# Kernel optimization log

Hardware: AMD Instinct MI355X
Metric: run time of the kernel (lower is better)

The kernel has to match this reference:

```python
import jax, jax.numpy as jnp
import numpy as np

N_HEAD = 16
LN_EPS = 1e-5


def _layernorm(x, g, b):
    mu = jnp.mean(x, axis=-1, keepdims=True)
    var = jnp.mean(jnp.square(x - mu), axis=-1, keepdims=True)
    return (x - mu) * jax.lax.rsqrt(var + LN_EPS) * g + b


def setup_inputs() -> dict:
    key = jax.random.key(0)
    ks = jax.random.split(key, 12)
    B, S, D = 2, 2048, 1024
    F = 4 * D
    std = 0.02
    return {
        "x": jax.random.normal(ks[0], (B, S, D), jnp.float32),
        "w_attn": jax.random.normal(ks[1], (D, 3 * D), jnp.float32) * std,
        "b_attn": jnp.zeros((3 * D,), jnp.float32),
        "w_o": jax.random.normal(ks[2], (D, D), jnp.float32) * std,
        "b_o": jnp.zeros((D,), jnp.float32),
        "ln1_g": jnp.ones((D,), jnp.float32),
        "ln1_b": jnp.zeros((D,), jnp.float32),
        "w_fc": jax.random.normal(ks[3], (D, F), jnp.float32) * std,
        "b_fc": jnp.zeros((F,), jnp.float32),
        "w_pr": jax.random.normal(ks[4], (F, D), jnp.float32) * std,
        "b_pr": jnp.zeros((D,), jnp.float32),
        "ln2_g": jnp.ones((D,), jnp.float32),
        "ln2_b": jnp.zeros((D,), jnp.float32),
    }


def reference(x, w_attn, b_attn, w_o, b_o, ln1_g, ln1_b,
              w_fc, b_fc, w_pr, b_pr, ln2_g, ln2_b):
    B, S, D = x.shape
    H = N_HEAD
    hd = D // H

    # --- attention ---
    qkv = x @ w_attn + b_attn                      # [B,S,3D]
    q, k, v = jnp.split(qkv, 3, axis=-1)
    q = q.reshape(B, S, H, hd).transpose(0, 2, 1, 3)  # [B,H,S,hd]
    k = k.reshape(B, S, H, hd).transpose(0, 2, 1, 3)
    v = v.reshape(B, S, H, hd).transpose(0, 2, 1, 3)

    # scores in fp32, scaled by sqrt(head_dim) (scale=True)
    w = jnp.einsum('bhqd,bhkd->bhqk', q.astype(jnp.float32),
                   k.astype(jnp.float32)) / jnp.sqrt(jnp.float32(hd))
    bias = jnp.tril(jnp.ones((S, S), jnp.float32))     # causal mask slice of registered buffer
    w = w * bias + (-10000.0) * (1.0 - bias)
    a = jax.nn.softmax(w, axis=-1).astype(v.dtype)
    o = jnp.einsum('bhqk,bhkd->bhqd', a, v)            # [B,H,S,hd]
    o = o.transpose(0, 2, 1, 3).reshape(B, S, D)
    a_out = o @ w_o + b_o

    # --- post-LN residual + MLP (gelu, d_ff = 4D) ---
    n = _layernorm(x + a_out, ln1_g, ln1_b)
    m = jax.nn.gelu(n @ w_fc + b_fc, approximate=False) @ w_pr + b_pr
    h = _layernorm(n + m, ln2_g, ln2_b)
    return h
```

## Files before the change

kernel.cpp:

```cpp
#include <hip/hip_runtime.h>
#include <stdint.h>
#include <math.h>


typedef __attribute__((ext_vector_type(4))) float f32x4;
typedef __attribute__((ext_vector_type(8))) short s16x8;

__device__ __forceinline__ float bf2f(short s){
  unsigned u = ((unsigned)(unsigned short)s) << 16;
  return __builtin_bit_cast(float, u);
}
__device__ __forceinline__ short f2bf(float f){
  unsigned u = __builtin_bit_cast(unsigned, f);
  unsigned r = (u + 0x7fffu + ((u >> 16) & 1u)) >> 16;
  return (short)(unsigned short)r;
}

__device__ __forceinline__ void gload_lds16(const void* gp, void* lp){
  __builtin_amdgcn_global_load_lds(
      (__attribute__((address_space(1))) void*)const_cast<void*>(gp),
      (__attribute__((address_space(3))) void*)lp,
      16, 0, 0);
}

__global__ void cvt_f32_bf16(const float* __restrict__ in, short* __restrict__ out, int n){
  int i = (blockIdx.x * blockDim.x + threadIdx.x) * 4;
  if (i < n){
    float4 v = *(const float4*)(in + i);
    short4 o;
    o.x = f2bf(v.x); o.y = f2bf(v.y); o.z = f2bf(v.z); o.w = f2bf(v.w);
    *(short4*)(out + i) = o;
  }
}

__global__ __launch_bounds__(256) void wtrans(const float* __restrict__ in,
                                              short* __restrict__ out, int R, int C){
  __shared__ float tile[32][33];
  int c0 = blockIdx.x * 32, r0 = blockIdx.y * 32;
  int tx = threadIdx.x, ty = threadIdx.y;
  #pragma unroll
  for (int j = 0; j < 4; ++j)
    tile[ty + j*8][tx] = in[(size_t)(r0 + ty + j*8) * C + c0 + tx];
  __syncthreads();
  #pragma unroll
  for (int j = 0; j < 4; ++j)
    out[(size_t)(c0 + ty + j*8) * R + r0 + tx] = f2bf(tile[tx][ty + j*8]);
}

__global__ __launch_bounds__(256) void vtrans(const short* __restrict__ qkv,
                                              short* __restrict__ vt){
  __shared__ short tile[32][33];
  int bh = blockIdx.z; int b = bh >> 4, h = bh & 15;
  int s0 = blockIdx.x * 32, d0 = blockIdx.y * 32;
  int tx = threadIdx.x, ty = threadIdx.y;
  #pragma unroll
  for (int j = 0; j < 4; ++j)
    tile[ty + j*8][tx] = qkv[(size_t)(b*2048 + s0 + ty + j*8) * 3072 + 2048 + h*64 + d0 + tx];
  __syncthreads();
  #pragma unroll
  for (int j = 0; j < 4; ++j)
    vt[(size_t)(bh*64 + d0 + ty + j*8) * 2048 + s0 + tx] = tile[tx][ty + j*8];
}

#define GBM 128
#define GBN 128
#define GBK 64

__global__ __launch_bounds__(256, 4) void gemm_bf16(
    const short* __restrict__ A, const short* __restrict__ BT,
    const float* __restrict__ bias,
    void* __restrict__ out, void* __restrict__ out2,
    void* __restrict__ out3, void* __restrict__ out4,
    int M, int N, int K, int EPI, int KS)
{
  __shared__ short sA[GBM * GBK];
  __shared__ short sB[GBN * GBK];
  const int t = threadIdx.x;
  const int lane = t & 63;
  const int w = t >> 6;
  const int wr = w >> 1, wc = w & 1;
  const int lrow = lane & 15;
  const int lk = lane >> 4;

  const int gx = gridDim.x;
  const int nwg = gx * gridDim.y;
  const int P = blockIdx.y * gx + blockIdx.x;
  const int wg = (P & 7) * (nwg >> 3) + (P >> 3);
  const int m0 = (wg / gx) * GBM, n0 = (wg % gx) * GBN;

  const int Kspl = K / KS;
  const int kbeg = blockIdx.z * Kspl;

  f32x4 acc[4][4] = {};

  for (int kk = kbeg; kk < kbeg + Kspl; kk += GBK){
    __syncthreads();
    #pragma unroll
    for (int r = 0; r < 4; ++r){
      int o = r * 4096 + t * 16;
      int row = o >> 7;
      int phys = (o >> 4) & 7;
      int lsl = phys ^ (row & 7);
      gload_lds16(A + (size_t)(m0 + row) * K + kk + lsl * 8, (char*)sA + o);
    }
    #pragma unroll
    for (int r = 0; r < 4; ++r){
      int o = r * 4096 + t * 16;
      int row = o >> 7;
      int phys = (o >> 4) & 7;
      int lsl = phys ^ (row & 7);
      gload_lds16(BT + (size_t)(n0 + row) * K + kk + lsl * 8, (char*)sB + o);
    }
    __syncthreads();

    #pragma unroll
    for (int kc = 0; kc < 2; ++kc){
      s16x8 af[4], bf[4];
      #pragma unroll
      for (int rt = 0; rt < 4; ++rt){
        int row = wr*64 + rt*16 + lrow;
        int slot = (kc*4 + lk) ^ (row & 7);
        af[rt] = *(const s16x8*)&sA[row*64 + slot*8];
      }
      #pragma unroll
      for (int ct = 0; ct < 4; ++ct){
        int row = wc*64 + ct*16 + lrow;
        int slot = (kc*4 + lk) ^ (row & 7);
        bf[ct] = *(const s16x8*)&sB[row*64 + slot*8];
      }
      #pragma unroll
      for (int rt = 0; rt < 4; ++rt)
        #pragma unroll
        for (int ct = 0; ct < 4; ++ct)
          acc[rt][ct] = __builtin_amdgcn_mfma_f32_16x16x32_bf16(af[rt], bf[ct], acc[rt][ct], 0, 0, 0);
    }
  }

  void* pz = (blockIdx.z == 0) ? out : (blockIdx.z == 1) ? out2
           : (blockIdx.z == 2) ? out3 : out4;
  #pragma unroll
  for (int rt = 0; rt < 4; ++rt){
    #pragma unroll
    for (int ct = 0; ct < 4; ++ct){
      #pragma unroll
      for (int r = 0; r < 4; ++r){
        int row = m0 + wr*64 + rt*16 + lk*4 + r;
        int col = n0 + wc*64 + ct*16 + lrow;
        size_t idx = (size_t)row * N + col;
        if (EPI == 4){
          ((short*)pz)[idx] = f2bf(acc[rt][ct][r]);
        } else {
          float v = acc[rt][ct][r] + bias[col];
          if (EPI == 0){
            ((short*)out)[idx] = f2bf(v);
          } else {
            float g = 0.5f * v * (1.0f + erff(v * 0.70710678118654752f));
            ((short*)out)[idx] = f2bf(g);
          }
        }
      }
    }
  }
}

__global__ __launch_bounds__(256, 2) void attn_kernel(
    const short* __restrict__ qkv, const short* __restrict__ vt,
    short* __restrict__ ob)
{
  const int P = blockIdx.x;
  const int xcd = P & 7;
  const int idx = P >> 3;
  const int pairi = idx & 15;
  const int bh = xcd + ((idx >> 4) << 3);
  const int b = bh >> 4, h = bh & 15;
  const int t  = threadIdx.x;
  const int lane = t & 63;
  const int w = t >> 6;
  const int lrow = lane & 15, lk = lane >> 4;

  __shared__ short sK[2][64*64];
  __shared__ short sV[2][64*64];
  __shared__ short sP[4][16][68];

  const size_t kgbase = (size_t)(b*2048)*3072 + 1024 + h*64;
  const size_t vgbase = (size_t)((b*16 + h)*64)*2048;

  s16x8 bones;
  #pragma unroll
  for (int i = 0; i < 8; ++i) bones[i] = (short)0x3F80;

  auto stage = [&](int buf, int k0){
    #pragma unroll
    for (int r2 = 0; r2 < 2; ++r2){
      int o = r2*4096 + t*16;
      int row = o >> 7;
      int lsl = ((o >> 4) & 7) ^ (row & 7);
      gload_lds16(qkv + kgbase + (size_t)(k0 + row)*3072 + lsl*8, (char*)sK[buf] + o);
      gload_lds16(vt  + vgbase + (size_t)row*2048 + k0   + lsl*8, (char*)sV[buf] + o);
    }
  };

  for (int pass = 0; pass < 2; ++pass){
    const int qt = pass ? 31 - pairi : pairi;
    const int q0 = qt * 64;
    const int qbase = q0 + w * 16;

    s16x8 aq[2];
    #pragma unroll
    for (int kc = 0; kc < 2; ++kc)
      aq[kc] = *(const s16x8*)(qkv + (size_t)(b*2048 + qbase + lrow)*3072 + h*64 + kc*32 + lk*8);

    f32x4 oacc[4] = {};
    f32x4 sumacc = {};

    const int nt = qt + 1;
    __syncthreads();
    stage(0, 0);
    __syncthreads();
    int cur = 0;

    for (int ktile = 0; ktile < nt; ++ktile){
      const int k0 = ktile * 64;
      if (ktile + 1 < nt) stage(cur ^ 1, k0 + 64);

      f32x4 sacc[4] = {};
      __builtin_amdgcn_s_setprio(1);
      #pragma unroll
      for (int kc = 0; kc < 2; ++kc){
        #pragma unroll
        for (int ct = 0; ct < 4; ++ct){
          int row = ct*16 + lrow;
          int slot = (kc*4 + lk) ^ (row & 7);
          s16x8 bk = *(const s16x8*)&sK[cur][row*64 + slot*8];
          sacc[ct] = __builtin_amdgcn_mfma_f32_16x16x32_bf16(aq[kc], bk, sacc[ct], 0, 0, 0);
        }
      }
      __builtin_amdgcn_s_setprio(0);

      const bool need_mask = (k0 + 63 > qbase);
      #pragma unroll
      for (int ct = 0; ct < 4; ++ct){
        #pragma unroll
        for (int r = 0; r < 4; ++r){
          float v = sacc[ct][r] * 0.125f;
          if (need_mask){
            int qi = qbase + lk*4 + r;
            int ki = k0 + ct*16 + lrow;
            if (ki > qi) v = -10000.0f;
          }
          sP[w][lk*4 + r][ct*16 + lrow] = f2bf(__expf(v));
        }
      }

      s16x8 pa[2];
      #pragma unroll
      for (int kc = 0; kc < 2; ++kc)
        pa[kc] = *(const s16x8*)&sP[w][lrow][kc*32 + lk*8];
      __builtin_amdgcn_s_setprio(1);
      #pragma unroll
      for (int dt = 0; dt < 4; ++dt){
        #pragma unroll
        for (int kc = 0; kc < 2; ++kc){
          int row = dt*16 + lrow;
          int slot = (kc*4 + lk) ^ (row & 7);
          s16x8 bv = *(const s16x8*)&sV[cur][row*64 + slot*8];
          oacc[dt] = __builtin_amdgcn_mfma_f32_16x16x32_bf16(pa[kc], bv, oacc[dt], 0, 0, 0);
        }
      }
      #pragma unroll
      for (int kc = 0; kc < 2; ++kc)
        sumacc = __builtin_amdgcn_mfma_f32_16x16x32_bf16(pa[kc], bones, sumacc, 0, 0, 0);
      __builtin_amdgcn_s_setprio(0);

      __syncthreads();
      cur ^= 1;
    }

    #pragma unroll
    for (int r = 0; r < 4; ++r){
      float inv = 1.0f / sumacc[r];
      int row = b*2048 + qbase + lk*4 + r;
      #pragma unroll
      for (int dt = 0; dt < 4; ++dt){
        int col = h*64 + dt*16 + lrow;
        ob[(size_t)row * 1024 + col] = f2bf(oacc[dt][r] * inv);
      }
    }
  }
}

__global__ __launch_bounds__(256) void ln_fused(
    const short* __restrict__ p0, const short* __restrict__ p1,
    const short* __restrict__ p2, const short* __restrict__ p3,
    const float* __restrict__ bias,
    const short* __restrict__ resid_bf, const float* __restrict__ resid_f,
    const float* __restrict__ g, const float* __restrict__ b,
    void* __restrict__ out, int bf16_out)
{
  const int row = blockIdx.x;
  const int t = threadIdx.x;
  const size_t base = (size_t)row*1024 + t*4;
  short4 a0 = *(const short4*)(p0 + base);
  short4 a1 = *(const short4*)(p1 + base);
  short4 a2 = *(const short4*)(p2 + base);
  short4 a3 = *(const short4*)(p3 + base);
  float4 bi = *(const float4*)(bias + t*4);
  float r0, r1, r2, r3;
  if (resid_bf){
    short4 rr = *(const short4*)(resid_bf + base);
    r0 = bf2f(rr.x); r1 = bf2f(rr.y); r2 = bf2f(rr.z); r3 = bf2f(rr.w);
  } else {
    float4 rr = *(const float4*)(resid_f + base);
    r0 = rr.x; r1 = rr.y; r2 = rr.z; r3 = rr.w;
  }
  float v0 = bf2f(a0.x) + bf2f(a1.x) + bf2f(a2.x) + bf2f(a3.x) + bi.x + r0;
  float v1 = bf2f(a0.y) + bf2f(a1.y) + bf2f(a2.y) + bf2f(a3.y) + bi.y + r1;
  float v2 = bf2f(a0.z) + bf2f(a1.z) + bf2f(a2.z) + bf2f(a3.z) + bi.z + r2;
  float v3 = bf2f(a0.w) + bf2f(a1.w) + bf2f(a2.w) + bf2f(a3.w) + bi.w + r3;
  float s = v0 + v1 + v2 + v3;
  float q = v0*v0 + v1*v1 + v2*v2 + v3*v3;
  #pragma unroll
  for (int off = 1; off < 64; off <<= 1){
    s += __shfl_xor(s, off, 64);
    q += __shfl_xor(q, off, 64);
  }
  __shared__ float ss[4], sq[4];
  if ((t & 63) == 0){ ss[t >> 6] = s; sq[t >> 6] = q; }
  __syncthreads();
  s = ss[0] + ss[1] + ss[2] + ss[3];
  q = sq[0] + sq[1] + sq[2] + sq[3];
  float mu = s * (1.0f/1024.0f);
  float var = q * (1.0f/1024.0f) - mu*mu;
  float rs = rsqrtf(var + 1e-5f);
  float4 gg = *(const float4*)(g + t*4);
  float4 bb = *(const float4*)(b + t*4);
  float o0 = (v0 - mu)*rs*gg.x + bb.x;
  float o1 = (v1 - mu)*rs*gg.y + bb.y;
  float o2 = (v2 - mu)*rs*gg.z + bb.z;
  float o3 = (v3 - mu)*rs*gg.w + bb.w;
  if (bf16_out){
    short4 o; o.x = f2bf(o0); o.y = f2bf(o1); o.z = f2bf(o2); o.w = f2bf(o3);
    *(short4*)((short*)out + base) = o;
  } else {
    float4 o = {o0, o1, o2, o3};
    *(float4*)((float*)out + base) = o;
  }
}

extern "C" void kernel_launch(void* const* d_in, const int* in_sizes, int n_in,
                              void* d_out, int out_size, void* d_ws, size_t ws_size,
                              hipStream_t stream) {
  const float* x      = (const float*)d_in[0];
  const float* w_attn = (const float*)d_in[1];
  const float* b_attn = (const float*)d_in[2];
  const float* w_o    = (const float*)d_in[3];
  const float* b_o    = (const float*)d_in[4];
  const float* ln1_g  = (const float*)d_in[5];
  const float* ln1_b  = (const float*)d_in[6];
  const float* w_fc   = (const float*)d_in[7];
  const float* b_fc   = (const float*)d_in[8];
  const float* w_pr   = (const float*)d_in[9];
  const float* b_pr   = (const float*)d_in[10];
  const float* ln2_g  = (const float*)d_in[11];
  const float* ln2_b  = (const float*)d_in[12];

  char* ws = (char*)d_ws;
  const size_t MB = 1048576;
  short* waT  = (short*)(ws + 0);
  short* wfT  = (short*)(ws + 6*MB);
  short* wpT  = (short*)(ws + 14*MB);
  short* woT  = (short*)(ws + 22*MB);
  short* xb   = (short*)(ws + 24*MB);
  short* vt   = (short*)(ws + 24*MB);
  short* pp2  = (short*)(ws + 24*MB);
  short* qkvb = (short*)(ws + 32*MB);
  short* fb   = (short*)(ws + 32*MB);
  short* ob   = (short*)(ws + 56*MB);
  short* pp0  = (short*)(ws + 64*MB);
  short* pp1  = (short*)(ws + 72*MB);
  short* nb   = (short*)(ws + 80*MB);
  short* pp3  = (short*)(ws + 88*MB);

  const int M = 4096;

  cvt_f32_bf16<<<dim3(M*1024/1024), dim3(256), 0, stream>>>(x, xb, M*1024);
  wtrans<<<dim3(3072/32, 1024/32), dim3(32,8), 0, stream>>>(w_attn, waT, 1024, 3072);
  wtrans<<<dim3(1024/32, 1024/32), dim3(32,8), 0, stream>>>(w_o,   woT, 1024, 1024);
  wtrans<<<dim3(4096/32, 1024/32), dim3(32,8), 0, stream>>>(w_fc,  wfT, 1024, 4096);
  wtrans<<<dim3(1024/32, 4096/32), dim3(32,8), 0, stream>>>(w_pr,  wpT, 4096, 1024);
  gemm_bf16<<<dim3(3072/GBN, M/GBM), dim3(256), 0, stream>>>(
      xb, waT, b_attn, qkvb, nullptr, nullptr, nullptr, M, 3072, 1024, 0, 1);
  vtrans<<<dim3(2048/32, 64/32, 32), dim3(32,8), 0, stream>>>(qkvb, vt);
  attn_kernel<<<dim3(512), dim3(256), 0, stream>>>(qkvb, vt, ob);
  gemm_bf16<<<dim3(1024/GBN, M/GBM, 4), dim3(256), 0, stream>>>(
      ob, woT, nullptr, pp0, pp1, pp2, pp3, M, 1024, 1024, 4, 4);
  ln_fused<<<dim3(M), dim3(256), 0, stream>>>(pp0, pp1, pp2, pp3, b_o,
                                              nullptr, x, ln1_g, ln1_b, nb, 1);
  gemm_bf16<<<dim3(4096/GBN, M/GBM), dim3(256), 0, stream>>>(
      nb, wfT, b_fc, fb, nullptr, nullptr, nullptr, M, 4096, 1024, 2, 1);
  gemm_bf16<<<dim3(1024/GBN, M/GBM, 4), dim3(256), 0, stream>>>(
      fb, wpT, nullptr, pp0, pp1, pp2, pp3, M, 1024, 4096, 4, 4);
  ln_fused<<<dim3(M), dim3(256), 0, stream>>>(pp0, pp1, pp2, pp3, b_pr,
                                              nb, nullptr, ln2_g, ln2_b, d_out, 0);
}
```

Baseline: 254.8 us.

## Double-buffer GEMM LDS tiles with K=32 stages and explicit waitcnt pipelining

Restructures the bf16 GEMM main loop into a two-stage double-buffered pipeline with K-tile 32. Each iteration issues global-to-LDS loads for the next tile, then waits only on the older loads before computing on the current one, so memory latency overlaps with MFMA work. It uses a new swizzled LDS layout with precomputed offsets, raised wave priority around the MFMA block, and explicit scheduling barriers. The cost is smaller K per iteration, which means more barriers and less MFMA work per synchronization, and hand-written vmcnt values that must match the number of loads issued.

```diff
diff --git a/kernel.cpp b/kernel.cpp
--- a/kernel.cpp
+++ b/kernel.cpp
@@ -64,7 +64,7 @@
 
 #define GBM 128
 #define GBN 128
-#define GBK 64
+#define TBK 32
 
 __global__ __launch_bounds__(256, 4) void gemm_bf16(
     const short* __restrict__ A, const short* __restrict__ BT,
@@ -73,8 +73,8 @@
     void* __restrict__ out3, void* __restrict__ out4,
     int M, int N, int K, int EPI, int KS)
 {
-  __shared__ short sA[GBM * GBK];
-  __shared__ short sB[GBN * GBK];
+  __shared__ __attribute__((aligned(16))) short sA[2][4096];
+  __shared__ __attribute__((aligned(16))) short sB[2][4096];
   const int t = threadIdx.x;
   const int lane = t & 63;
   const int w = t >> 6;
@@ -90,50 +90,72 @@
 
   const int Kspl = K / KS;
   const int kbeg = blockIdx.z * Kspl;
+  const int NT = Kspl / TBK;
+
+  const short* gA[2]; const short* gB[2]; int ldo[2];
+  #pragma unroll
+  for (int q = 0; q < 2; ++q){
+    int o = q*4096 + t*16;
+    int line = o >> 7, h = (o >> 6) & 1, s = (o >> 4) & 3;
+    int row = line*2 + h;
+    int ck = s ^ (line & 3);
+    ldo[q] = o;
+    gA[q] = A  + (size_t)(m0 + row) * K + kbeg + ck*8;
+    gB[q] = BT + (size_t)(n0 + row) * K + kbeg + ck*8;
+  }
+
+  int aoff[4], boff[4];
+  #pragma unroll
+  for (int m = 0; m < 4; ++m){
+    int row = wr*64 + m*16 + lrow, line = row >> 1;
+    aoff[m] = line*64 + (row & 1)*32 + (lk ^ (line & 3))*8;
+  }
+  #pragma unroll
+  for (int n = 0; n < 4; ++n){
+    int row = wc*64 + n*16 + lrow, line = row >> 1;
+    boff[n] = line*64 + (row & 1)*32 + (lk ^ (line & 3))*8;
+  }
+
+  auto stage = [&](int buf, int tt){
+    const int ko = tt * TBK;
+    #pragma unroll
+    for (int q = 0; q < 2; ++q){
+      gload_lds16(gA[q] + ko, (char*)&sA[buf][0] + ldo[q]);
+      gload_lds16(gB[q] + ko, (char*)&sB[buf][0] + ldo[q]);
+    }
+  };
 
   f32x4 acc[4][4] = {};
 
-  for (int kk = kbeg; kk < kbeg + Kspl; kk += GBK){
-    __syncthreads();
-    #pragma unroll
-    for (int r = 0; r < 4; ++r){
-      int o = r * 4096 + t * 16;
-      int row = o >> 7;
-      int phys = (o >> 4) & 7;
-      int lsl = phys ^ (row & 7);
-      gload_lds16(A + (size_t)(m0 + row) * K + kk + lsl * 8, (char*)sA + o);
-    }
-    #pragma unroll
-    for (int r = 0; r < 4; ++r){
-      int o = r * 4096 + t * 16;
-      int row = o >> 7;
-      int phys = (o >> 4) & 7;
-      int lsl = phys ^ (row & 7);
-      gload_lds16(BT + (size_t)(n0 + row) * K + kk + lsl * 8, (char*)sB + o);
-    }
-    __syncthreads();
-
-    #pragma unroll
-    for (int kc = 0; kc < 2; ++kc){
-      s16x8 af[4], bf[4];
-      #pragma unroll
-      for (int rt = 0; rt < 4; ++rt){
-        int row = wr*64 + rt*16 + lrow;
-        int slot = (kc*4 + lk) ^ (row & 7);
-        af[rt] = *(const s16x8*)&sA[row*64 + slot*8];
-      }
-      #pragma unroll
-      for (int ct = 0; ct < 4; ++ct){
-        int row = wc*64 + ct*16 + lrow;
-        int slot = (kc*4 + lk) ^ (row & 7);
-        bf[ct] = *(const s16x8*)&sB[row*64 + slot*8];
-      }
-      #pragma unroll
-      for (int rt = 0; rt < 4; ++rt)
-        #pragma unroll
-        for (int ct = 0; ct < 4; ++ct)
-          acc[rt][ct] = __builtin_amdgcn_mfma_f32_16x16x32_bf16(af[rt], bf[ct], acc[rt][ct], 0, 0, 0);
-    }
+  stage(0, 0);
+  for (int tt = 0; tt < NT; ++tt){
+    if (tt + 1 < NT){
+      stage((tt + 1) & 1, tt + 1);
+      asm volatile("s_waitcnt vmcnt(4)" ::: "memory");
+    } else {
+      asm volatile("s_waitcnt vmcnt(0)" ::: "memory");
+    }
+    __builtin_amdgcn_s_barrier();
+    __builtin_amdgcn_sched_barrier(0);
+
+    const short* pa = &sA[tt & 1][0];
+    const short* pb = &sB[tt & 1][0];
+    s16x8 af[4], bf[4];
+    #pragma unroll
+    for (int m = 0; m < 4; ++m) af[m] = *(const s16x8*)(pa + aoff[m]);
+    #pragma unroll
+    for (int n = 0; n < 4; ++n) bf[n] = *(const s16x8*)(pb + boff[n]);
+    asm volatile("s_waitcnt lgkmcnt(0)" ::: "memory");
+    __builtin_amdgcn_sched_barrier(0);
+    __builtin_amdgcn_s_setprio(1);
+    #pragma unroll
+    for (int m = 0; m < 4; ++m)
+      #pragma unroll
+      for (int n = 0; n < 4; ++n)
+        acc[m][n] = __builtin_amdgcn_mfma_f32_16x16x32_bf16(af[m], bf[n], acc[m][n], 0, 0, 0);
+    __builtin_amdgcn_s_setprio(0);
+    __builtin_amdgcn_sched_barrier(0);
+    __builtin_amdgcn_s_barrier();
   }
 
   void* pz = (blockIdx.z == 0) ? out : (blockIdx.z == 1) ? out2
```

Result: slower. 262.2 us (+2.9%).

## Split attention key range across two blocks and add a combine kernel

Applied to the files above, without the earlier changes.

Each attention work item (a query-tile pair for one head) is now split into two blocks, each covering half of the causal key tiles. The grid doubles to 1024 blocks and the occupancy hint rises to 3 blocks per SM. Each half writes an unnormalised bf16 partial output and its row sums. A new combine kernel adds the two partials and divides by the summed normalisers. The aim is more parallelism and better load balance on the attention step, at the cost of an extra kernel launch, extra global traffic, and an additional bf16 rounding of the partial outputs.

```diff
diff --git a/kernel.cpp b/kernel.cpp
--- a/kernel.cpp
+++ b/kernel.cpp
@@ -163,20 +163,25 @@
   }
 }
 
-__global__ __launch_bounds__(256, 2) void attn_kernel(
+__global__ __launch_bounds__(256, 3) void attn_kernel(
     const short* __restrict__ qkv, const short* __restrict__ vt,
-    short* __restrict__ ob)
+    short* __restrict__ oa0, short* __restrict__ oa1,
+    float* __restrict__ sums0, float* __restrict__ sums1)
 {
   const int P = blockIdx.x;
   const int xcd = P & 7;
   const int idx = P >> 3;
-  const int pairi = idx & 15;
-  const int bh = xcd + ((idx >> 4) << 3);
+  const int ks = idx & 1;
+  const int pairi = (idx >> 1) & 15;
+  const int bh = xcd + ((idx >> 5) << 3);
   const int b = bh >> 4, h = bh & 15;
   const int t  = threadIdx.x;
   const int lane = t & 63;
   const int w = t >> 6;
   const int lrow = lane & 15, lk = lane >> 4;
+
+  short* oa = ks ? oa1 : oa0;
+  float* sums = ks ? sums1 : sums0;
 
   __shared__ short sK[2][64*64];
   __shared__ short sV[2][64*64];
@@ -205,6 +210,11 @@
     const int q0 = qt * 64;
     const int qbase = q0 + w * 16;
 
+    const int nt = qt + 1;
+    const int half = (nt + 1) >> 1;
+    const int kstart = ks ? half : 0;
+    const int kend   = ks ? nt : half;
+
     s16x8 aq[2];
     #pragma unroll
     for (int kc = 0; kc < 2; ++kc)
@@ -213,15 +223,14 @@
     f32x4 oacc[4] = {};
     f32x4 sumacc = {};
 
-    const int nt = qt + 1;
     __syncthreads();
-    stage(0, 0);
+    if (kend > kstart) stage(0, kstart * 64);
     __syncthreads();
     int cur = 0;
 
-    for (int ktile = 0; ktile < nt; ++ktile){
+    for (int ktile = kstart; ktile < kend; ++ktile){
       const int k0 = ktile * 64;
-      if (ktile + 1 < nt) stage(cur ^ 1, k0 + 64);
+      if (ktile + 1 < kend) stage(cur ^ 1, k0 + 64);
 
       f32x4 sacc[4] = {};
       __builtin_amdgcn_s_setprio(1);
@@ -278,15 +287,36 @@
 
     #pragma unroll
     for (int r = 0; r < 4; ++r){
-      float inv = 1.0f / sumacc[r];
       int row = b*2048 + qbase + lk*4 + r;
       #pragma unroll
       for (int dt = 0; dt < 4; ++dt){
         int col = h*64 + dt*16 + lrow;
-        ob[(size_t)row * 1024 + col] = f2bf(oacc[dt][r] * inv);
-      }
-    }
-  }
+        oa[(size_t)row * 1024 + col] = f2bf(oacc[dt][r]);
+      }
+      if (lrow == 0) sums[row*16 + h] = sumacc[r];
+    }
+  }
+}
+
+__global__ __launch_bounds__(256) void attn_combine(
+    const short* __restrict__ oa0, const short* __restrict__ oa1,
+    const float* __restrict__ sums0, const float* __restrict__ sums1,
+    short* __restrict__ ob)
+{
+  const int row = blockIdx.x;
+  const int t = threadIdx.x;
+  const int col = t * 4;
+  const int h = col >> 6;
+  const float inv = 1.0f / (sums0[row*16 + h] + sums1[row*16 + h]);
+  const size_t base = (size_t)row*1024 + col;
+  short4 a = *(const short4*)(oa0 + base);
+  short4 c = *(const short4*)(oa1 + base);
+  short4 o;
+  o.x = f2bf((bf2f(a.x) + bf2f(c.x)) * inv);
+  o.y = f2bf((bf2f(a.y) + bf2f(c.y)) * inv);
+  o.z = f2bf((bf2f(a.z) + bf2f(c.z)) * inv);
+  o.w = f2bf((bf2f(a.w) + bf2f(c.w)) * inv);
+  *(short4*)(ob + base) = o;
 }
 
 __global__ __launch_bounds__(256) void ln_fused(
@@ -367,6 +397,8 @@
   char* ws = (char*)d_ws;
   const size_t MB = 1048576;
   short* waT  = (short*)(ws + 0);
+  float* sums0= (float*)(ws + 0);
+  float* sums1= (float*)(ws + 1*MB);
   short* wfT  = (short*)(ws + 6*MB);
   short* wpT  = (short*)(ws + 14*MB);
   short* woT  = (short*)(ws + 22*MB);
@@ -376,7 +408,9 @@
   short* qkvb = (short*)(ws + 32*MB);
   short* fb   = (short*)(ws + 32*MB);
   short* ob   = (short*)(ws + 56*MB);
+  short* oa0  = (short*)(ws + 64*MB);
   short* pp0  = (short*)(ws + 64*MB);
+  short* oa1  = (short*)(ws + 72*MB);
   short* pp1  = (short*)(ws + 72*MB);
   short* nb   = (short*)(ws + 80*MB);
   short* pp3  = (short*)(ws + 88*MB);
@@ -391,7 +425,8 @@
   gemm_bf16<<<dim3(3072/GBN, M/GBM), dim3(256), 0, stream>>>(
       xb, waT, b_attn, qkvb, nullptr, nullptr, nullptr, M, 3072, 1024, 0, 1);
   vtrans<<<dim3(2048/32, 64/32, 32), dim3(32,8), 0, stream>>>(qkvb, vt);
-  attn_kernel<<<dim3(512), dim3(256), 0, stream>>>(qkvb, vt, ob);
+  attn_kernel<<<dim3(1024), dim3(256), 0, stream>>>(qkvb, vt, oa0, oa1, sums0, sums1);
+  attn_combine<<<dim3(M), dim3(256), 0, stream>>>(oa0, oa1, sums0, sums1, ob);
   gemm_bf16<<<dim3(1024/GBN, M/GBM, 4), dim3(256), 0, stream>>>(
       ob, woT, nullptr, pp0, pp1, pp2, pp3, M, 1024, 1024, 4, 4);
   ln_fused<<<dim3(M), dim3(256), 0, stream>>>(pp0, pp1, pp2, pp3, b_o,
```

New measurement: 262.5 us. 3.0% more time.

## Fuse paired causal query tiles into one K/V sweep in attention kernel

Applied to the files above, without the earlier changes.

Each attention block used to handle its two query tiles (qt and 31-qt) in two separate passes, loading K/V twice for the overlapping prefix. Now both tiles are processed in a single loop over the longer tile's K/V range, and the short tile also computes on the shared staged tiles while ktile < ntA. This roughly halves K/V staging for the short tile and removes one pipeline restart. It also reverses the pairi order for some groups to spread work across blocks. The cost is doubled accumulator registers, which may pressure occupancy under launch_bounds(256,2).

```diff
diff --git a/kernel.cpp b/kernel.cpp
--- a/kernel.cpp
+++ b/kernel.cpp
@@ -170,8 +170,10 @@
   const int P = blockIdx.x;
   const int xcd = P & 7;
   const int idx = P >> 3;
-  const int pairi = idx & 15;
-  const int bh = xcd + ((idx >> 4) << 3);
+  const int raw = idx & 15;
+  const int grp = idx >> 4;
+  const int pairi = (grp & 2) ? (15 - raw) : raw;
+  const int bh = xcd + (grp << 3);
   const int b = bh >> 4, h = bh & 15;
   const int t  = threadIdx.x;
   const int lane = t & 63;
@@ -200,29 +202,32 @@
     }
   };
 
-  for (int pass = 0; pass < 2; ++pass){
-    const int qt = pass ? 31 - pairi : pairi;
-    const int q0 = qt * 64;
-    const int qbase = q0 + w * 16;
-
-    s16x8 aq[2];
-    #pragma unroll
-    for (int kc = 0; kc < 2; ++kc)
-      aq[kc] = *(const s16x8*)(qkv + (size_t)(b*2048 + qbase + lrow)*3072 + h*64 + kc*32 + lk*8);
-
-    f32x4 oacc[4] = {};
-    f32x4 sumacc = {};
-
-    const int nt = qt + 1;
-    __syncthreads();
-    stage(0, 0);
-    __syncthreads();
-    int cur = 0;
-
-    for (int ktile = 0; ktile < nt; ++ktile){
-      const int k0 = ktile * 64;
-      if (ktile + 1 < nt) stage(cur ^ 1, k0 + 64);
-
+  const int qtA = pairi;
+  const int qtB = 31 - pairi;
+  const int qbaseA = qtA*64 + w*16;
+  const int qbaseB = qtB*64 + w*16;
+
+  s16x8 aqA[2], aqB[2];
+  #pragma unroll
+  for (int kc = 0; kc < 2; ++kc){
+    aqA[kc] = *(const s16x8*)(qkv + (size_t)(b*2048 + qbaseA + lrow)*3072 + h*64 + kc*32 + lk*8);
+    aqB[kc] = *(const s16x8*)(qkv + (size_t)(b*2048 + qbaseB + lrow)*3072 + h*64 + kc*32 + lk*8);
+  }
+
+  f32x4 oaccA[4] = {}, oaccB[4] = {};
+  f32x4 sumA = {}, sumB = {};
+
+  const int ntA = qtA + 1;
+  const int ntB = qtB + 1;
+  stage(0, 0);
+  __syncthreads();
+  int cur = 0;
+
+  for (int ktile = 0; ktile < ntB; ++ktile){
+    const int k0 = ktile * 64;
+    if (ktile + 1 < ntB) stage(cur ^ 1, k0 + 64);
+
+    {
       f32x4 sacc[4] = {};
       __builtin_amdgcn_s_setprio(1);
       #pragma unroll
@@ -232,19 +237,19 @@
           int row = ct*16 + lrow;
           int slot = (kc*4 + lk) ^ (row & 7);
           s16x8 bk = *(const s16x8*)&sK[cur][row*64 + slot*8];
-          sacc[ct] = __builtin_amdgcn_mfma_f32_16x16x32_bf16(aq[kc], bk, sacc[ct], 0, 0, 0);
+          sacc[ct] = __builtin_amdgcn_mfma_f32_16x16x32_bf16(aqB[kc], bk, sacc[ct], 0, 0, 0);
         }
       }
       __builtin_amdgcn_s_setprio(0);
 
-      const bool need_mask = (k0 + 63 > qbase);
+      const bool need_mask = (k0 + 63 > qbaseB);
       #pragma unroll
       for (int ct = 0; ct < 4; ++ct){
         #pragma unroll
         for (int r = 0; r < 4; ++r){
           float v = sacc[ct][r] * 0.125f;
           if (need_mask){
-            int qi = qbase + lk*4 + r;
+            int qi = qbaseB + lk*4 + r;
             int ki = k0 + ct*16 + lrow;
             if (ki > qi) v = -10000.0f;
           }
@@ -264,27 +269,81 @@
           int row = dt*16 + lrow;
           int slot = (kc*4 + lk) ^ (row & 7);
           s16x8 bv = *(const s16x8*)&sV[cur][row*64 + slot*8];
-          oacc[dt] = __builtin_amdgcn_mfma_f32_16x16x32_bf16(pa[kc], bv, oacc[dt], 0, 0, 0);
+          oaccB[dt] = __builtin_amdgcn_mfma_f32_16x16x32_bf16(pa[kc], bv, oaccB[dt], 0, 0, 0);
         }
       }
       #pragma unroll
       for (int kc = 0; kc < 2; ++kc)
-        sumacc = __builtin_amdgcn_mfma_f32_16x16x32_bf16(pa[kc], bones, sumacc, 0, 0, 0);
+        sumB = __builtin_amdgcn_mfma_f32_16x16x32_bf16(pa[kc], bones, sumB, 0, 0, 0);
       __builtin_amdgcn_s_setprio(0);
-
-      __syncthreads();
-      cur ^= 1;
-    }
-
-    #pragma unroll
-    for (int r = 0; r < 4; ++r){
-      float inv = 1.0f / sumacc[r];
-      int row = b*2048 + qbase + lk*4 + r;
+    }
+
+    if (ktile < ntA){
+      f32x4 sacc[4] = {};
+      __builtin_amdgcn_s_setprio(1);
+      #pragma unroll
+      for (int kc = 0; kc < 2; ++kc){
+        #pragma unroll
+        for (int ct = 0; ct < 4; ++ct){
+          int row = ct*16 + lrow;
+          int slot = (kc*4 + lk) ^ (row & 7);
+          s16x8 bk = *(const s16x8*)&sK[cur][row*64 + slot*8];
+          sacc[ct] = __builtin_amdgcn_mfma_f32_16x16x32_bf16(aqA[kc], bk, sacc[ct], 0, 0, 0);
+        }
+      }
+      __builtin_amdgcn_s_setprio(0);
+
+      const bool need_mask = (k0 + 63 > qbaseA);
+      #pragma unroll
+      for (int ct = 0; ct < 4; ++ct){
+        #pragma unroll
+        for (int r = 0; r < 4; ++r){
+          float v = sacc[ct][r] * 0.125f;
+          if (need_mask){
+            int qi = qbaseA + lk*4 + r;
+            int ki = k0 + ct*16 + lrow;
+            if (ki > qi) v = -10000.0f;
+          }
+          sP[w][lk*4 + r][ct*16 + lrow] = f2bf(__expf(v));
+        }
+      }
+
+      s16x8 pa[2];
+      #pragma unroll
+      for (int kc = 0; kc < 2; ++kc)
+        pa[kc] = *(const s16x8*)&sP[w][lrow][kc*32 + lk*8];
+      __builtin_amdgcn_s_setprio(1);
       #pragma unroll
       for (int dt = 0; dt < 4; ++dt){
-        int col = h*64 + dt*16 + lrow;
-        ob[(size_t)row * 1024 + col] = f2bf(oacc[dt][r] * inv);
-      }
+        #pragma unroll
+        for (int kc = 0; kc < 2; ++kc){
+          int row = dt*16 + lrow;
+          int slot = (kc*4 + lk) ^ (row & 7);
+          s16x8 bv = *(const s16x8*)&sV[cur][row*64 + slot*8];
+          oaccA[dt] = __builtin_amdgcn_mfma_f32_16x16x32_bf16(pa[kc], bv, oaccA[dt], 0, 0, 0);
+        }
+      }
+      #pragma unroll
+      for (int kc = 0; kc < 2; ++kc)
+        sumA = __builtin_amdgcn_mfma_f32_16x16x32_bf16(pa[kc], bones, sumA, 0, 0, 0);
+      __builtin_amdgcn_s_setprio(0);
+    }
+
+    __syncthreads();
+    cur ^= 1;
+  }
+
+  #pragma unroll
+  for (int r = 0; r < 4; ++r){
+    float invA = 1.0f / sumA[r];
+    float invB = 1.0f / sumB[r];
+    int rowA = b*2048 + qbaseA + lk*4 + r;
+    int rowB = b*2048 + qbaseB + lk*4 + r;
+    #pragma unroll
+    for (int dt = 0; dt < 4; ++dt){
+      int col = h*64 + dt*16 + lrow;
+      ob[(size_t)rowA * 1024 + col] = f2bf(oaccA[dt][r] * invA);
+      ob[(size_t)rowB * 1024 + col] = f2bf(oaccB[dt][r] * invB);
     }
   }
 }
```

Result: no change. 254.7 us (-0.1%).
